# Kernel tuning notes

Measured on AMD Instinct MI355X. Metric: run time of the kernel, lower is better.

## Reference

```python
import jax, jax.numpy as jnp
import numpy as np

NUM_HEADS = 16
EMBED_DIM = 1024
HEAD_DIM = EMBED_DIM // NUM_HEADS


def setup_inputs() -> dict:
    key = jax.random.key(0)
    kq, kk, kv, kw, kb = jax.random.split(key, 5)
    B, S, D = 2, 2048, EMBED_DIM
    bound = 1.0 / np.sqrt(D)
    return {
        "query": jax.random.normal(kq, (B, S, D), dtype=jnp.float32),
        "key": jax.random.normal(kk, (B, S, D), dtype=jnp.float32),
        "value": jax.random.normal(kv, (B, S, D), dtype=jnp.float32),
        "W_out": jax.random.uniform(kw, (D, D), minval=-bound, maxval=bound, dtype=jnp.float32),
        "b_out": jax.random.uniform(kb, (D,), minval=-bound, maxval=bound, dtype=jnp.float32),
        "prelu_a": jnp.array(0.25, dtype=jnp.float32),
    }


def reference(query, key, value, W_out, b_out, prelu_a):
    B, S, D = query.shape
    # Note: the original forward never applies q/k/v linear layers, only reshape.
    q = query.reshape(B, S, NUM_HEADS, HEAD_DIM)  # b s h d
    k = key.reshape(B, S, NUM_HEADS, HEAD_DIM)
    v = value.reshape(B, S, NUM_HEADS, HEAD_DIM)
    scale = 1.0 / np.sqrt(HEAD_DIM).astype(np.float32)
    scores = jnp.einsum("bqhd,bkhd->bhqk", q, k) * scale  # [B,H,S,S]
    attn = jax.nn.softmax(scores, axis=-1)
    out = jnp.einsum("bhqk,bkhd->bqhd", attn, v).reshape(B, S, D)
    out = out @ W_out.T + b_out  # torch Linear: x @ W.T + b
    # dropout is identity in eval mode; PReLU with single scalar param
    out = jnp.where(out >= 0, out, prelu_a * out)
    return out
```

## Files before the change

kernel.cpp:

```cpp
#include <hip/hip_runtime.h>
#include <hip/hip_bf16.h>

typedef __attribute__((ext_vector_type(8))) short bf16x8;
typedef __attribute__((ext_vector_type(4))) float f32x4;

#define S_LEN 2048
#define EMB   1024
#define NH    16
#define HD    64

__device__ inline int swz(int row, int chunk) {
  return row * 64 + ((chunk ^ (row & 7)) << 3);
}

__device__ inline int swz128(int row, int chunk) {
  return row * 128 + ((chunk ^ (row & 15)) << 3);
}

__device__ inline int kperm(int s) {
  return (s & 0x23) | ((s & 0x04) << 2) | ((s & 0x18) >> 1);
}

__device__ inline uint4 cvt8(const float* __restrict__ src, float scale) {
  float4 f0 = ((const float4*)src)[0];
  float4 f1 = ((const float4*)src)[1];
  __hip_bfloat16 t[8];
  t[0] = __float2bfloat16(f0.x * scale);
  t[1] = __float2bfloat16(f0.y * scale);
  t[2] = __float2bfloat16(f0.z * scale);
  t[3] = __float2bfloat16(f0.w * scale);
  t[4] = __float2bfloat16(f1.x * scale);
  t[5] = __float2bfloat16(f1.y * scale);
  t[6] = __float2bfloat16(f1.z * scale);
  t[7] = __float2bfloat16(f1.w * scale);
  return *(uint4*)t;
}

__device__ inline uint4 cvt8r(float4 f0, float4 f1) {
  __hip_bfloat16 t[8];
  t[0] = __float2bfloat16(f0.x);
  t[1] = __float2bfloat16(f0.y);
  t[2] = __float2bfloat16(f0.z);
  t[3] = __float2bfloat16(f0.w);
  t[4] = __float2bfloat16(f1.x);
  t[5] = __float2bfloat16(f1.y);
  t[6] = __float2bfloat16(f1.z);
  t[7] = __float2bfloat16(f1.w);
  return *(uint4*)t;
}

__device__ inline void ld8f(const float* __restrict__ p, float4& a, float4& b) {
  a = ((const float4*)p)[0];
  b = ((const float4*)p)[1];
}

__global__ __launch_bounds__(256)
void prep(const float* __restrict__ K, const float* __restrict__ V,
          __hip_bfloat16* __restrict__ Kb, __hip_bfloat16* __restrict__ Vt) {
  __shared__ float vt[64 * 65];
  const int tid = threadIdx.x;
  const int st = blockIdx.x, h = blockIdx.y, b = blockIdx.z;
  const size_t srcbase = ((size_t)(b * S_LEN + st * 64)) * EMB + h * HD;
  const size_t kvb = ((size_t)(b * NH + h) * S_LEN + st * 64) * HD;
  const size_t vtb = ((size_t)(b * NH + h) * HD) * S_LEN + st * 64;

  for (int c = tid; c < 512; c += 256) {
    const int r = c >> 3, c8 = (c & 7) * 8;
    *(uint4*)(Kb + kvb + r * HD + c8) = cvt8(K + srcbase + (size_t)r * EMB + c8, 1.0f);
    const float* vsrc = V + srcbase + (size_t)r * EMB + c8;
    float4 a = ((const float4*)vsrc)[0];
    float4 d4 = ((const float4*)vsrc)[1];
    float tv[8] = {a.x, a.y, a.z, a.w, d4.x, d4.y, d4.z, d4.w};
    #pragma unroll
    for (int j = 0; j < 8; ++j) vt[r * 65 + c8 + j] = tv[j];
  }
  __syncthreads();
  for (int c = tid; c < 512; c += 256) {
    const int d = c >> 3, s8 = (c & 7) * 8;
    __hip_bfloat16 t[8];
    #pragma unroll
    for (int j = 0; j < 8; ++j)
      t[j] = __float2bfloat16(vt[(s8 + j) * 65 + d]);
    *(uint4*)(Vt + vtb + (size_t)d * S_LEN + s8) = *(uint4*)t;
  }
}

__global__ __launch_bounds__(512, 4)
void attn_fwd(const float* __restrict__ Q,
              const __hip_bfloat16* __restrict__ Kb,
              const __hip_bfloat16* __restrict__ Vt,
              __hip_bfloat16* __restrict__ O)
{
  __shared__ __align__(16) __hip_bfloat16 qs[128 * 64];
  __shared__ __align__(16) __hip_bfloat16 ks[2][128 * 64];
  __shared__ __align__(16) __hip_bfloat16 vs[2][64 * 128];

  const int qt   = blockIdx.x;
  const int h    = blockIdx.y;
  const int b    = blockIdx.z;
  const int tid  = threadIdx.x;
  const int wave = tid >> 6;
  const int lane = tid & 63;
  const int ln   = lane & 15;
  const int qd   = lane >> 4;

  const size_t baseQ = ((size_t)(b * S_LEN + qt * 128)) * EMB + h * HD;
  const size_t kvb   = ((size_t)(b * NH + h) * S_LEN) * HD;
  const size_t vtb   = ((size_t)(b * NH + h) * HD) * S_LEN;

  const int r0 = tid >> 3, cc = tid & 7;
  const int kpos0 = swz(kperm(r0), cc);
  const int kpos1 = kpos0 + 64 * 64;
  const int vr0 = tid >> 4, vch = tid & 15;
  const int vpos0 = swz128(vr0, vch);
  const int vpos1 = vpos0 + 32 * 128;

  uint4 kreg0 = *(const uint4*)(Kb + kvb + (size_t)(r0)       * HD + cc * 8);
  uint4 kreg1 = *(const uint4*)(Kb + kvb + (size_t)(64 + r0)  * HD + cc * 8);
  uint4 vreg0 = *(const uint4*)(Vt + vtb + (size_t)vr0        * S_LEN + vch * 8);
  uint4 vreg1 = *(const uint4*)(Vt + vtb + (size_t)(vr0 + 32) * S_LEN + vch * 8);

  const float qscale = 0.125f * 1.44269504088896f;
  #pragma unroll
  for (int i = 0; i < 2; ++i) {
    const int c = tid + 512 * i, row = c >> 3, ch = c & 7;
    *(uint4*)&qs[swz(row, ch)] = cvt8(Q + baseQ + (size_t)row * EMB + ch * 8, qscale);
  }
  *(uint4*)&ks[0][kpos0] = kreg0;
  *(uint4*)&ks[0][kpos1] = kreg1;
  *(uint4*)&vs[0][vpos0] = vreg0;
  *(uint4*)&vs[0][vpos1] = vreg1;
  kreg0 = *(const uint4*)(Kb + kvb + (size_t)(128 + r0)      * HD + cc * 8);
  kreg1 = *(const uint4*)(Kb + kvb + (size_t)(192 + r0)      * HD + cc * 8);
  vreg0 = *(const uint4*)(Vt + vtb + (size_t)vr0        * S_LEN + 128 + vch * 8);
  vreg1 = *(const uint4*)(Vt + vtb + (size_t)(vr0 + 32) * S_LEN + 128 + vch * 8);
  __syncthreads();

  bf16x8 aq[2];
  #pragma unroll
  for (int kh = 0; kh < 2; ++kh)
    aq[kh] = *(const bf16x8*)&qs[swz(wave * 16 + ln, kh * 4 + qd)];

  bf16x8 ones;
  #pragma unroll
  for (int j = 0; j < 8; ++j) ones[j] = (short)0x3F80;

  f32x4 oacc[4] = {};
  f32x4 lacc = {};
  bf16x8 apD[2] = {};
  bf16x8 bvD[8] = {};

  for (int kt = 0; kt < S_LEN / 128; ++kt) {
    const int cur = kt & 1;
    if (kt + 1 < S_LEN / 128) {
      *(uint4*)&ks[1 - cur][kpos0] = kreg0;
      *(uint4*)&ks[1 - cur][kpos1] = kreg1;
      *(uint4*)&vs[1 - cur][vpos0] = vreg0;
      *(uint4*)&vs[1 - cur][vpos1] = vreg1;
      if (kt + 2 < S_LEN / 128) {
        const int kb2 = (kt + 2) * 128;
        kreg0 = *(const uint4*)(Kb + kvb + (size_t)(kb2 + r0)       * HD + cc * 8);
        kreg1 = *(const uint4*)(Kb + kvb + (size_t)(kb2 + 64 + r0)  * HD + cc * 8);
        vreg0 = *(const uint4*)(Vt + vtb + (size_t)vr0        * S_LEN + kb2 + vch * 8);
        vreg1 = *(const uint4*)(Vt + vtb + (size_t)(vr0 + 32) * S_LEN + kb2 + vch * 8);
      }
    }

    f32x4 sfA[4];
    __builtin_amdgcn_s_setprio(1);
    #pragma unroll
    for (int k16 = 0; k16 < 4; ++k16) {
      const int krow = k16 * 16 + ln;
      bf16x8 ak0 = *(const bf16x8*)&ks[cur][swz(krow, qd)];
      bf16x8 ak1 = *(const bf16x8*)&ks[cur][swz(krow, 4 + qd)];
      f32x4 acc = {};
      acc = __builtin_amdgcn_mfma_f32_16x16x32_bf16(ak0, aq[0], acc, 0, 0, 0);
      sfA[k16] = __builtin_amdgcn_mfma_f32_16x16x32_bf16(ak1, aq[1], acc, 0, 0, 0);
    }
    __builtin_amdgcn_s_setprio(0);

    bf16x8 apA[2];
    #pragma unroll
    for (int t2 = 0; t2 < 2; ++t2)
      #pragma unroll
      for (int j = 0; j < 8; ++j) {
        const float p = __builtin_amdgcn_exp2f(sfA[t2 * 2 + (j >> 2)][j & 3]);
        __hip_bfloat16 hb = __float2bfloat16(p);
        apA[t2][j] = *(short*)&hb;
      }

    f32x4 sfB[4];
    __builtin_amdgcn_s_setprio(1);
    #pragma unroll
    for (int t = 0; t < 2; ++t) {
      lacc = __builtin_amdgcn_mfma_f32_16x16x32_bf16(apD[t], ones, lacc, 0, 0, 0);
      #pragma unroll
      for (int dn = 0; dn < 4; ++dn)
        oacc[dn] = __builtin_amdgcn_mfma_f32_16x16x32_bf16(apD[t], bvD[t * 4 + dn], oacc[dn], 0, 0, 0);
    }
    #pragma unroll
    for (int k16 = 0; k16 < 4; ++k16) {
      const int krow = (4 + k16) * 16 + ln;
      bf16x8 ak0 = *(const bf16x8*)&ks[cur][swz(krow, qd)];
      bf16x8 ak1 = *(const bf16x8*)&ks[cur][swz(krow, 4 + qd)];
      f32x4 acc = {};
      acc = __builtin_amdgcn_mfma_f32_16x16x32_bf16(ak0, aq[0], acc, 0, 0, 0);
      sfB[k16] = __builtin_amdgcn_mfma_f32_16x16x32_bf16(ak1, aq[1], acc, 0, 0, 0);
    }
    __builtin_amdgcn_s_setprio(0);

    bf16x8 apB[2];
    #pragma unroll
    for (int t2 = 0; t2 < 2; ++t2)
      #pragma unroll
      for (int j = 0; j < 8; ++j) {
        const float p = __builtin_amdgcn_exp2f(sfB[t2 * 2 + (j >> 2)][j & 3]);
        __hip_bfloat16 hb = __float2bfloat16(p);
        apB[t2][j] = *(short*)&hb;
      }

    __builtin_amdgcn_s_setprio(1);
    #pragma unroll
    for (int t = 0; t < 2; ++t) {
      lacc = __builtin_amdgcn_mfma_f32_16x16x32_bf16(apA[t], ones, lacc, 0, 0, 0);
      #pragma unroll
      for (int dn = 0; dn < 4; ++dn) {
        bf16x8 bv = *(const bf16x8*)&vs[cur][swz128(dn * 16 + ln, t * 4 + qd)];
        oacc[dn] = __builtin_amdgcn_mfma_f32_16x16x32_bf16(apA[t], bv, oacc[dn], 0, 0, 0);
      }
    }
    __builtin_amdgcn_s_setprio(0);

    #pragma unroll
    for (int t = 0; t < 2; ++t)
      #pragma unroll
      for (int dn = 0; dn < 4; ++dn)
        bvD[t * 4 + dn] = *(const bf16x8*)&vs[cur][swz128(dn * 16 + ln, (2 + t) * 4 + qd)];
    apD[0] = apB[0];
    apD[1] = apB[1];

    __syncthreads();
  }

  #pragma unroll
  for (int t = 0; t < 2; ++t) {
    lacc = __builtin_amdgcn_mfma_f32_16x16x32_bf16(apD[t], ones, lacc, 0, 0, 0);
    #pragma unroll
    for (int dn = 0; dn < 4; ++dn)
      oacc[dn] = __builtin_amdgcn_mfma_f32_16x16x32_bf16(apD[t], bvD[t * 4 + dn], oacc[dn], 0, 0, 0);
  }
  #pragma unroll
  for (int r = 0; r < 4; ++r) {
    const float inv = 1.f / lacc[r];
    const int row = wave * 16 + qd * 4 + r;
    #pragma unroll
    for (int dn = 0; dn < 4; ++dn)
      O[baseQ + (size_t)row * EMB + dn * 16 + ln] =
          __float2bfloat16(oacc[dn][r] * inv);
  }
}

__global__ __launch_bounds__(256, 2)
void proj_prelu(const __hip_bfloat16* __restrict__ X,
                const float* __restrict__ W,
                const float* __restrict__ Bv,
                const float* __restrict__ Pa,
                float* __restrict__ Out)
{
  __shared__ __align__(16) __hip_bfloat16 xs[2][128 * 64];
  __shared__ __align__(16) __hip_bfloat16 wsm[2][64 * 64];

  const int m0   = blockIdx.x * 128;
  const int n0   = blockIdx.y * 64;
  const int tid  = threadIdx.x;
  const int wave = tid >> 6;
  const int wm   = wave >> 1;
  const int wn   = wave & 1;
  const int lane = tid & 63;
  const int ln   = lane & 15;
  const int qd   = lane >> 4;

  const int r0 = tid >> 3, cc = tid & 7;

  f32x4 acc[8] = {};

  uint4 xg0, xg1, xg2, xg3;
  float4 wa0, wb0, wa1, wb1;
  #define LOADK(ko)                                                           \
    xg0 = *(const uint4*)(X  + (size_t)(m0 + r0     ) * EMB + (ko) + cc * 8); \
    xg1 = *(const uint4*)(X  + (size_t)(m0 + r0 + 32) * EMB + (ko) + cc * 8); \
    xg2 = *(const uint4*)(X  + (size_t)(m0 + r0 + 64) * EMB + (ko) + cc * 8); \
    xg3 = *(const uint4*)(X  + (size_t)(m0 + r0 + 96) * EMB + (ko) + cc * 8); \
    ld8f(W + (size_t)(n0 + r0     ) * EMB + (ko) + cc * 8, wa0, wb0);         \
    ld8f(W + (size_t)(n0 + r0 + 32) * EMB + (ko) + cc * 8, wa1, wb1)
  #define STORELDS(buf)                                                       \
    *(uint4*)&xs [buf][swz(r0,      cc)] = xg0;                               \
    *(uint4*)&xs [buf][swz(r0 + 32, cc)] = xg1;                               \
    *(uint4*)&xs [buf][swz(r0 + 64, cc)] = xg2;                               \
    *(uint4*)&xs [buf][swz(r0 + 96, cc)] = xg3;                               \
    *(uint4*)&wsm[buf][swz(r0,      cc)] = cvt8r(wa0, wb0);                   \
    *(uint4*)&wsm[buf][swz(r0 + 32, cc)] = cvt8r(wa1, wb1)

  LOADK(0);
  STORELDS(0);
  LOADK(64);
  __syncthreads();

  for (int kt = 0; kt < EMB / 64; ++kt) {
    const int cur = kt & 1;
    if (kt + 1 < EMB / 64) {
      STORELDS(1 - cur);
      if (kt + 2 < EMB / 64) {
        LOADK((kt + 2) * 64);
      }
    }

    #pragma unroll
    for (int ks2 = 0; ks2 < 2; ++ks2) {
      bf16x8 ax0 = *(const bf16x8*)&xs[cur][swz(wm * 64 +  0 + ln, ks2 * 4 + qd)];
      bf16x8 ax1 = *(const bf16x8*)&xs[cur][swz(wm * 64 + 16 + ln, ks2 * 4 + qd)];
      bf16x8 ax2 = *(const bf16x8*)&xs[cur][swz(wm * 64 + 32 + ln, ks2 * 4 + qd)];
      bf16x8 ax3 = *(const bf16x8*)&xs[cur][swz(wm * 64 + 48 + ln, ks2 * 4 + qd)];
      bf16x8 bw0 = *(const bf16x8*)&wsm[cur][swz(wn * 32 +  0 + ln, ks2 * 4 + qd)];
      bf16x8 bw1 = *(const bf16x8*)&wsm[cur][swz(wn * 32 + 16 + ln, ks2 * 4 + qd)];
      acc[0] = __builtin_amdgcn_mfma_f32_16x16x32_bf16(ax0, bw0, acc[0], 0, 0, 0);
      acc[1] = __builtin_amdgcn_mfma_f32_16x16x32_bf16(ax0, bw1, acc[1], 0, 0, 0);
      acc[2] = __builtin_amdgcn_mfma_f32_16x16x32_bf16(ax1, bw0, acc[2], 0, 0, 0);
      acc[3] = __builtin_amdgcn_mfma_f32_16x16x32_bf16(ax1, bw1, acc[3], 0, 0, 0);
      acc[4] = __builtin_amdgcn_mfma_f32_16x16x32_bf16(ax2, bw0, acc[4], 0, 0, 0);
      acc[5] = __builtin_amdgcn_mfma_f32_16x16x32_bf16(ax2, bw1, acc[5], 0, 0, 0);
      acc[6] = __builtin_amdgcn_mfma_f32_16x16x32_bf16(ax3, bw0, acc[6], 0, 0, 0);
      acc[7] = __builtin_amdgcn_mfma_f32_16x16x32_bf16(ax3, bw1, acc[7], 0, 0, 0);
    }
    __syncthreads();
  }

  const float a = Pa[0];
  #pragma unroll
  for (int mf = 0; mf < 4; ++mf) {
    #pragma unroll
    for (int nf = 0; nf < 2; ++nf) {
      const float bn = Bv[n0 + wn * 32 + nf * 16 + ln];
      #pragma unroll
      for (int r = 0; r < 4; ++r) {
        float y = acc[mf * 2 + nf][r] + bn;
        y = (y >= 0.f) ? y : a * y;
        Out[(size_t)(m0 + wm * 64 + mf * 16 + qd * 4 + r) * EMB +
            n0 + wn * 32 + nf * 16 + ln] = y;
      }
    }
  }
  #undef LOADK
  #undef STORELDS
}

extern "C" void kernel_launch(void* const* d_in, const int* in_sizes, int n_in,
                              void* d_out, int out_size, void* d_ws, size_t ws_size,
                              hipStream_t stream) {
  const float* Q  = (const float*)d_in[0];
  const float* K  = (const float*)d_in[1];
  const float* V  = (const float*)d_in[2];
  const float* W  = (const float*)d_in[3];
  const float* Bb = (const float*)d_in[4];
  const float* Pa = (const float*)d_in[5];
  float* Out = (float*)d_out;

  char* ws = (char*)d_ws;
  __hip_bfloat16* Xws = (__hip_bfloat16*)(ws);
  __hip_bfloat16* Kb  = (__hip_bfloat16*)(ws + (8u  << 20));
  __hip_bfloat16* Vt  = (__hip_bfloat16*)(ws + (16u << 20));

  prep      <<<dim3(S_LEN / 64, NH, 2), 256, 0, stream>>>(K, V, Kb, Vt);
  attn_fwd  <<<dim3(S_LEN / 128, NH, 2), 512, 0, stream>>>(Q, Kb, Vt, Xws);
  proj_prelu<<<dim3(2 * S_LEN / 128, EMB / 64), 256, 0, stream>>>(Xws, W, Bb, Pa, Out);
}
```

Baseline: 155.9 us.

## Fuse prep, attention and projection into one cooperative persistent kernel

Replaces the three launches with a single cooperative kernel of 512 blocks. It runs K/V conversion, then flash attention, then the output projection with PReLU, separated by grid-wide syncs, and keeps the old three-kernel path as a fallback if the cooperative launch fails. The attention loop drops the software-pipelined deferred PV stage in favour of a plain in-order schedule, and the projection retiles to 8 waves over a 128x64 tile. This aims to remove launch gaps and tail effects, but adds grid sync costs and a 512-thread projection phase with less work per wave.

```diff
diff --git a/kernel.cpp b/kernel.cpp
--- a/kernel.cpp
+++ b/kernel.cpp
@@ -1,5 +1,8 @@
 #include <hip/hip_runtime.h>
 #include <hip/hip_bf16.h>
+#include <hip/hip_cooperative_groups.h>
+
+namespace cg = cooperative_groups;
 
 typedef __attribute__((ext_vector_type(8))) short bf16x8;
 typedef __attribute__((ext_vector_type(4))) float f32x4;
@@ -54,6 +57,286 @@
   b = ((const float4*)p)[1];
 }
 
+__global__ __launch_bounds__(512, 4)
+void fused_mha(const float* __restrict__ Q, const float* __restrict__ K,
+               const float* __restrict__ V, const float* __restrict__ W,
+               const float* __restrict__ Bv, const float* __restrict__ Pa,
+               __hip_bfloat16* __restrict__ Kb, __hip_bfloat16* __restrict__ Vt,
+               __hip_bfloat16* __restrict__ X, float* __restrict__ Out)
+{
+  __shared__ __align__(16) char smem[81920];
+  cg::grid_group grid = cg::this_grid();
+
+  const int bid = blockIdx.x;
+  const int tid = threadIdx.x;
+
+  {
+    float* vt = (float*)smem;
+    #pragma unroll
+    for (int ui = 0; ui < 2; ++ui) {
+      const int u = bid + ui * 512;
+      const int st = u & 31, h = (u >> 5) & 15, b = u >> 9;
+      const size_t srcbase = ((size_t)(b * S_LEN + st * 64)) * EMB + h * HD;
+      const size_t kvbp = ((size_t)(b * NH + h) * S_LEN + st * 64) * HD;
+      const size_t vtbp = ((size_t)(b * NH + h) * HD) * S_LEN + st * 64;
+
+      const int r = tid >> 3, c8 = (tid & 7) * 8;
+      *(uint4*)(Kb + kvbp + r * HD + c8) =
+          cvt8(K + srcbase + (size_t)r * EMB + c8, 1.0f);
+      const float* vsrc = V + srcbase + (size_t)r * EMB + c8;
+      float4 a = ((const float4*)vsrc)[0];
+      float4 d4 = ((const float4*)vsrc)[1];
+      float tv[8] = {a.x, a.y, a.z, a.w, d4.x, d4.y, d4.z, d4.w};
+      #pragma unroll
+      for (int j = 0; j < 8; ++j) vt[r * 65 + c8 + j] = tv[j];
+      __syncthreads();
+      const int d = tid >> 3, s8 = (tid & 7) * 8;
+      __hip_bfloat16 t[8];
+      #pragma unroll
+      for (int j = 0; j < 8; ++j)
+        t[j] = __float2bfloat16(vt[(s8 + j) * 65 + d]);
+      *(uint4*)(Vt + vtbp + (size_t)d * S_LEN + s8) = *(uint4*)t;
+      __syncthreads();
+    }
+  }
+
+  __threadfence();
+  grid.sync();
+
+  {
+    __hip_bfloat16* qs  = (__hip_bfloat16*)smem;
+    __hip_bfloat16* ksb = (__hip_bfloat16*)(smem + 16384);
+    __hip_bfloat16* vsb = (__hip_bfloat16*)(smem + 49152);
+
+    const int qt = bid & 15;
+    const int h  = (bid >> 4) & 15;
+    const int b  = bid >> 8;
+    const int wave = tid >> 6;
+    const int lane = tid & 63;
+    const int ln   = lane & 15;
+    const int qd   = lane >> 4;
+
+    const size_t baseQ = ((size_t)(b * S_LEN + qt * 128)) * EMB + h * HD;
+    const size_t kvb   = ((size_t)(b * NH + h) * S_LEN) * HD;
+    const size_t vtb   = ((size_t)(b * NH + h) * HD) * S_LEN;
+
+    const int r0 = tid >> 3, cc = tid & 7;
+    const int kpos0 = swz(kperm(r0), cc);
+    const int kpos1 = kpos0 + 64 * 64;
+    const int vr0 = tid >> 4, vch = tid & 15;
+    const int vpos0 = swz128(vr0, vch);
+    const int vpos1 = vpos0 + 32 * 128;
+
+    uint4 kreg0 = *(const uint4*)(Kb + kvb + (size_t)(r0)       * HD + cc * 8);
+    uint4 kreg1 = *(const uint4*)(Kb + kvb + (size_t)(64 + r0)  * HD + cc * 8);
+    uint4 vreg0 = *(const uint4*)(Vt + vtb + (size_t)vr0        * S_LEN + vch * 8);
+    uint4 vreg1 = *(const uint4*)(Vt + vtb + (size_t)(vr0 + 32) * S_LEN + vch * 8);
+
+    const float qscale = 0.125f * 1.44269504088896f;
+    #pragma unroll
+    for (int i = 0; i < 2; ++i) {
+      const int c = tid + 512 * i, row = c >> 3, ch = c & 7;
+      *(uint4*)&qs[swz(row, ch)] = cvt8(Q + baseQ + (size_t)row * EMB + ch * 8, qscale);
+    }
+    *(uint4*)&ksb[kpos0] = kreg0;
+    *(uint4*)&ksb[kpos1] = kreg1;
+    *(uint4*)&vsb[vpos0] = vreg0;
+    *(uint4*)&vsb[vpos1] = vreg1;
+    kreg0 = *(const uint4*)(Kb + kvb + (size_t)(128 + r0)      * HD + cc * 8);
+    kreg1 = *(const uint4*)(Kb + kvb + (size_t)(192 + r0)      * HD + cc * 8);
+    vreg0 = *(const uint4*)(Vt + vtb + (size_t)vr0        * S_LEN + 128 + vch * 8);
+    vreg1 = *(const uint4*)(Vt + vtb + (size_t)(vr0 + 32) * S_LEN + 128 + vch * 8);
+    __syncthreads();
+
+    bf16x8 aq[2];
+    #pragma unroll
+    for (int kh = 0; kh < 2; ++kh)
+      aq[kh] = *(const bf16x8*)&qs[swz(wave * 16 + ln, kh * 4 + qd)];
+
+    bf16x8 ones;
+    #pragma unroll
+    for (int j = 0; j < 8; ++j) ones[j] = (short)0x3F80;
+
+    f32x4 oacc[4] = {};
+    f32x4 lacc = {};
+
+    for (int kt = 0; kt < S_LEN / 128; ++kt) {
+      const int cur = kt & 1;
+      __hip_bfloat16* ksc = ksb + cur * (128 * 64);
+      __hip_bfloat16* vsc = vsb + cur * (64 * 128);
+      __hip_bfloat16* ksn = ksb + (1 - cur) * (128 * 64);
+      __hip_bfloat16* vsn = vsb + (1 - cur) * (64 * 128);
+      if (kt + 1 < S_LEN / 128) {
+        *(uint4*)&ksn[kpos0] = kreg0;
+        *(uint4*)&ksn[kpos1] = kreg1;
+        *(uint4*)&vsn[vpos0] = vreg0;
+        *(uint4*)&vsn[vpos1] = vreg1;
+        if (kt + 2 < S_LEN / 128) {
+          const int kb2 = (kt + 2) * 128;
+          kreg0 = *(const uint4*)(Kb + kvb + (size_t)(kb2 + r0)       * HD + cc * 8);
+          kreg1 = *(const uint4*)(Kb + kvb + (size_t)(kb2 + 64 + r0)  * HD + cc * 8);
+          vreg0 = *(const uint4*)(Vt + vtb + (size_t)vr0        * S_LEN + kb2 + vch * 8);
+          vreg1 = *(const uint4*)(Vt + vtb + (size_t)(vr0 + 32) * S_LEN + kb2 + vch * 8);
+        }
+      }
+
+      f32x4 sfA[4], sfB[4];
+      __builtin_amdgcn_s_setprio(1);
+      #pragma unroll
+      for (int k16 = 0; k16 < 4; ++k16) {
+        const int krow = k16 * 16 + ln;
+        bf16x8 ak0 = *(const bf16x8*)&ksc[swz(krow, qd)];
+        bf16x8 ak1 = *(const bf16x8*)&ksc[swz(krow, 4 + qd)];
+        f32x4 acc = {};
+        acc = __builtin_amdgcn_mfma_f32_16x16x32_bf16(ak0, aq[0], acc, 0, 0, 0);
+        sfA[k16] = __builtin_amdgcn_mfma_f32_16x16x32_bf16(ak1, aq[1], acc, 0, 0, 0);
+      }
+      #pragma unroll
+      for (int k16 = 0; k16 < 4; ++k16) {
+        const int krow = (4 + k16) * 16 + ln;
+        bf16x8 ak0 = *(const bf16x8*)&ksc[swz(krow, qd)];
+        bf16x8 ak1 = *(const bf16x8*)&ksc[swz(krow, 4 + qd)];
+        f32x4 acc = {};
+        acc = __builtin_amdgcn_mfma_f32_16x16x32_bf16(ak0, aq[0], acc, 0, 0, 0);
+        sfB[k16] = __builtin_amdgcn_mfma_f32_16x16x32_bf16(ak1, aq[1], acc, 0, 0, 0);
+      }
+      __builtin_amdgcn_s_setprio(0);
+
+      bf16x8 apA[2];
+      #pragma unroll
+      for (int t2 = 0; t2 < 2; ++t2)
+        #pragma unroll
+        for (int j = 0; j < 8; ++j) {
+          const float p = __builtin_amdgcn_exp2f(sfA[t2 * 2 + (j >> 2)][j & 3]);
+          __hip_bfloat16 hb = __float2bfloat16(p);
+          apA[t2][j] = *(short*)&hb;
+        }
+
+      __builtin_amdgcn_s_setprio(1);
+      #pragma unroll
+      for (int t = 0; t < 2; ++t) {
+        lacc = __builtin_amdgcn_mfma_f32_16x16x32_bf16(apA[t], ones, lacc, 0, 0, 0);
+        #pragma unroll
+        for (int dn = 0; dn < 4; ++dn) {
+          bf16x8 bv = *(const bf16x8*)&vsc[swz128(dn * 16 + ln, t * 4 + qd)];
+          oacc[dn] = __builtin_amdgcn_mfma_f32_16x16x32_bf16(apA[t], bv, oacc[dn], 0, 0, 0);
+        }
+      }
+      __builtin_amdgcn_s_setprio(0);
+
+      bf16x8 apB[2];
+      #pragma unroll
+      for (int t2 = 0; t2 < 2; ++t2)
+        #pragma unroll
+        for (int j = 0; j < 8; ++j) {
+          const float p = __builtin_amdgcn_exp2f(sfB[t2 * 2 + (j >> 2)][j & 3]);
+          __hip_bfloat16 hb = __float2bfloat16(p);
+          apB[t2][j] = *(short*)&hb;
+        }
+
+      __builtin_amdgcn_s_setprio(1);
+      #pragma unroll
+      for (int t = 0; t < 2; ++t) {
+        lacc = __builtin_amdgcn_mfma_f32_16x16x32_bf16(apB[t], ones, lacc, 0, 0, 0);
+        #pragma unroll
+        for (int dn = 0; dn < 4; ++dn) {
+          bf16x8 bv = *(const bf16x8*)&vsc[swz128(dn * 16 + ln, (2 + t) * 4 + qd)];
+          oacc[dn] = __builtin_amdgcn_mfma_f32_16x16x32_bf16(apB[t], bv, oacc[dn], 0, 0, 0);
+        }
+      }
+      __builtin_amdgcn_s_setprio(0);
+
+      __syncthreads();
+    }
+
+    #pragma unroll
+    for (int r = 0; r < 4; ++r) {
+      const float inv = 1.f / lacc[r];
+      const int row = wave * 16 + qd * 4 + r;
+      #pragma unroll
+      for (int dn = 0; dn < 4; ++dn)
+        X[baseQ + (size_t)row * EMB + dn * 16 + ln] =
+            __float2bfloat16(oacc[dn][r] * inv);
+    }
+  }
+
+  __threadfence();
+  grid.sync();
+
+  {
+    __hip_bfloat16* xs  = (__hip_bfloat16*)smem;
+    __hip_bfloat16* wsm = (__hip_bfloat16*)(smem + 32768);
+
+    const int m0 = (bid & 31) * 128;
+    const int n0 = (bid >> 5) * 64;
+    const int wave = tid >> 6;
+    const int wm = wave >> 2;
+    const int wq = wave & 3;
+    const int lane = tid & 63;
+    const int ln   = lane & 15;
+    const int qd   = lane >> 4;
+    const int r0 = tid >> 3, cc = tid & 7;
+
+    f32x4 acc[4] = {};
+
+    uint4 xg0, xg1;
+    float4 wa0, wb0;
+    #define LOADK(ko)                                                            \
+      xg0 = *(const uint4*)(X + (size_t)(m0 + r0     ) * EMB + (ko) + cc * 8);   \
+      xg1 = *(const uint4*)(X + (size_t)(m0 + r0 + 64) * EMB + (ko) + cc * 8);   \
+      ld8f(W + (size_t)(n0 + r0) * EMB + (ko) + cc * 8, wa0, wb0)
+    #define STORELDS(buf)                                                        \
+      *(uint4*)&xs [(buf) * 8192 + swz(r0,      cc)] = xg0;                      \
+      *(uint4*)&xs [(buf) * 8192 + swz(r0 + 64, cc)] = xg1;                      \
+      *(uint4*)&wsm[(buf) * 4096 + swz(r0,      cc)] = cvt8r(wa0, wb0)
+
+    LOADK(0);
+    STORELDS(0);
+    LOADK(64);
+    __syncthreads();
+
+    for (int kt = 0; kt < EMB / 64; ++kt) {
+      const int cur = kt & 1;
+      if (kt + 1 < EMB / 64) {
+        STORELDS(1 - cur);
+        if (kt + 2 < EMB / 64) {
+          LOADK((kt + 2) * 64);
+        }
+      }
+      const __hip_bfloat16* xc = xs + cur * 8192;
+      const __hip_bfloat16* wc = wsm + cur * 4096;
+      #pragma unroll
+      for (int ks2 = 0; ks2 < 2; ++ks2) {
+        bf16x8 ax0 = *(const bf16x8*)&xc[swz(wm * 64 +  0 + ln, ks2 * 4 + qd)];
+        bf16x8 ax1 = *(const bf16x8*)&xc[swz(wm * 64 + 16 + ln, ks2 * 4 + qd)];
+        bf16x8 ax2 = *(const bf16x8*)&xc[swz(wm * 64 + 32 + ln, ks2 * 4 + qd)];
+        bf16x8 ax3 = *(const bf16x8*)&xc[swz(wm * 64 + 48 + ln, ks2 * 4 + qd)];
+        bf16x8 bw  = *(const bf16x8*)&wc[swz(wq * 16 + ln, ks2 * 4 + qd)];
+        acc[0] = __builtin_amdgcn_mfma_f32_16x16x32_bf16(ax0, bw, acc[0], 0, 0, 0);
+        acc[1] = __builtin_amdgcn_mfma_f32_16x16x32_bf16(ax1, bw, acc[1], 0, 0, 0);
+        acc[2] = __builtin_amdgcn_mfma_f32_16x16x32_bf16(ax2, bw, acc[2], 0, 0, 0);
+        acc[3] = __builtin_amdgcn_mfma_f32_16x16x32_bf16(ax3, bw, acc[3], 0, 0, 0);
+      }
+      __syncthreads();
+    }
+
+    const float a = Pa[0];
+    const float bn = Bv[n0 + wq * 16 + ln];
+    #pragma unroll
+    for (int mf = 0; mf < 4; ++mf) {
+      #pragma unroll
+      for (int r = 0; r < 4; ++r) {
+        float y = acc[mf][r] + bn;
+        y = (y >= 0.f) ? y : a * y;
+        Out[(size_t)(m0 + wm * 64 + mf * 16 + qd * 4 + r) * EMB +
+            n0 + wq * 16 + ln] = y;
+      }
+    }
+    #undef LOADK
+    #undef STORELDS
+  }
+}
+
 __global__ __launch_bounds__(256)
 void prep(const float* __restrict__ K, const float* __restrict__ V,
           __hip_bfloat16* __restrict__ Kb, __hip_bfloat16* __restrict__ Vt) {
@@ -95,14 +378,9 @@
   __shared__ __align__(16) __hip_bfloat16 ks[2][128 * 64];
   __shared__ __align__(16) __hip_bfloat16 vs[2][64 * 128];
 
-  const int qt   = blockIdx.x;
-  const int h    = blockIdx.y;
-  const int b    = blockIdx.z;
-  const int tid  = threadIdx.x;
-  const int wave = tid >> 6;
-  const int lane = tid & 63;
-  const int ln   = lane & 15;
-  const int qd   = lane >> 4;
+  const int qt = blockIdx.x, h = blockIdx.y, b = blockIdx.z;
+  const int tid = threadIdx.x;
+  const int wave = tid >> 6, lane = tid & 63, ln = lane & 15, qd = lane >> 4;
 
   const size_t baseQ = ((size_t)(b * S_LEN + qt * 128)) * EMB + h * HD;
   const size_t kvb   = ((size_t)(b * NH + h) * S_LEN) * HD;
@@ -147,8 +425,6 @@
 
   f32x4 oacc[4] = {};
   f32x4 lacc = {};
-  bf16x8 apD[2] = {};
-  bf16x8 bvD[8] = {};
 
   for (int kt = 0; kt < S_LEN / 128; ++kt) {
     const int cur = kt & 1;
@@ -166,7 +442,7 @@
       }
     }
 
-    f32x4 sfA[4];
+    f32x4 sfA[4], sfB[4];
     __builtin_amdgcn_s_setprio(1);
     #pragma unroll
     for (int k16 = 0; k16 < 4; ++k16) {
@@ -177,27 +453,6 @@
       acc = __builtin_amdgcn_mfma_f32_16x16x32_bf16(ak0, aq[0], acc, 0, 0, 0);
       sfA[k16] = __builtin_amdgcn_mfma_f32_16x16x32_bf16(ak1, aq[1], acc, 0, 0, 0);
     }
-    __builtin_amdgcn_s_setprio(0);
-
-    bf16x8 apA[2];
-    #pragma unroll
-    for (int t2 = 0; t2 < 2; ++t2)
-      #pragma unroll
-      for (int j = 0; j < 8; ++j) {
-        const float p = __builtin_amdgcn_exp2f(sfA[t2 * 2 + (j >> 2)][j & 3]);
-        __hip_bfloat16 hb = __float2bfloat16(p);
-        apA[t2][j] = *(short*)&hb;
-      }
-
-    f32x4 sfB[4];
-    __builtin_amdgcn_s_setprio(1);
-    #pragma unroll
-    for (int t = 0; t < 2; ++t) {
-      lacc = __builtin_amdgcn_mfma_f32_16x16x32_bf16(apD[t], ones, lacc, 0, 0, 0);
-      #pragma unroll
-      for (int dn = 0; dn < 4; ++dn)
-        oacc[dn] = __builtin_amdgcn_mfma_f32_16x16x32_bf16(apD[t], bvD[t * 4 + dn], oacc[dn], 0, 0, 0);
-    }
     #pragma unroll
     for (int k16 = 0; k16 < 4; ++k16) {
       const int krow = (4 + k16) * 16 + ln;
@@ -209,6 +464,28 @@
     }
     __builtin_amdgcn_s_setprio(0);
 
+    bf16x8 apA[2];
+    #pragma unroll
+    for (int t2 = 0; t2 < 2; ++t2)
+      #pragma unroll
+      for (int j = 0; j < 8; ++j) {
+        const float p = __builtin_amdgcn_exp2f(sfA[t2 * 2 + (j >> 2)][j & 3]);
+        __hip_bfloat16 hb = __float2bfloat16(p);
+        apA[t2][j] = *(short*)&hb;
+      }
+
+    __builtin_amdgcn_s_setprio(1);
+    #pragma unroll
+    for (int t = 0; t < 2; ++t) {
+      lacc = __builtin_amdgcn_mfma_f32_16x16x32_bf16(apA[t], ones, lacc, 0, 0, 0);
+      #pragma unroll
+      for (int dn = 0; dn < 4; ++dn) {
+        bf16x8 bv = *(const bf16x8*)&vs[cur][swz128(dn * 16 + ln, t * 4 + qd)];
+        oacc[dn] = __builtin_amdgcn_mfma_f32_16x16x32_bf16(apA[t], bv, oacc[dn], 0, 0, 0);
+      }
+    }
+    __builtin_amdgcn_s_setprio(0);
+
     bf16x8 apB[2];
     #pragma unroll
     for (int t2 = 0; t2 < 2; ++t2)
@@ -222,33 +499,18 @@
     __builtin_amdgcn_s_setprio(1);
     #pragma unroll
     for (int t = 0; t < 2; ++t) {
-      lacc = __builtin_amdgcn_mfma_f32_16x16x32_bf16(apA[t], ones, lacc, 0, 0, 0);
+      lacc = __builtin_amdgcn_mfma_f32_16x16x32_bf16(apB[t], ones, lacc, 0, 0, 0);
       #pragma unroll
       for (int dn = 0; dn < 4; ++dn) {
-        bf16x8 bv = *(const bf16x8*)&vs[cur][swz128(dn * 16 + ln, t * 4 + qd)];
-        oacc[dn] = __builtin_amdgcn_mfma_f32_16x16x32_bf16(apA[t], bv, oacc[dn], 0, 0, 0);
+        bf16x8 bv = *(const bf16x8*)&vs[cur][swz128(dn * 16 + ln, (2 + t) * 4 + qd)];
+        oacc[dn] = __builtin_amdgcn_mfma_f32_16x16x32_bf16(apB[t], bv, oacc[dn], 0, 0, 0);
       }
     }
     __builtin_amdgcn_s_setprio(0);
 
-    #pragma unroll
-    for (int t = 0; t < 2; ++t)
-      #pragma unroll
-      for (int dn = 0; dn < 4; ++dn)
-        bvD[t * 4 + dn] = *(const bf16x8*)&vs[cur][swz128(dn * 16 + ln, (2 + t) * 4 + qd)];
-    apD[0] = apB[0];
-    apD[1] = apB[1];
-
     __syncthreads();
   }
 
-  #pragma unroll
-  for (int t = 0; t < 2; ++t) {
-    lacc = __builtin_amdgcn_mfma_f32_16x16x32_bf16(apD[t], ones, lacc, 0, 0, 0);
-    #pragma unroll
-    for (int dn = 0; dn < 4; ++dn)
-      oacc[dn] = __builtin_amdgcn_mfma_f32_16x16x32_bf16(apD[t], bvD[t * 4 + dn], oacc[dn], 0, 0, 0);
-  }
   #pragma unroll
   for (int r = 0; r < 4; ++r) {
     const float inv = 1.f / lacc[r];
@@ -270,16 +532,12 @@
   __shared__ __align__(16) __hip_bfloat16 xs[2][128 * 64];
   __shared__ __align__(16) __hip_bfloat16 wsm[2][64 * 64];
 
-  const int m0   = blockIdx.x * 128;
-  const int n0   = blockIdx.y * 64;
-  const int tid  = threadIdx.x;
+  const int m0 = blockIdx.x * 128;
+  const int n0 = blockIdx.y * 64;
+  const int tid = threadIdx.x;
   const int wave = tid >> 6;
-  const int wm   = wave >> 1;
-  const int wn   = wave & 1;
-  const int lane = tid & 63;
-  const int ln   = lane & 15;
-  const int qd   = lane >> 4;
-
+  const int wm = wave >> 1, wn = wave & 1;
+  const int lane = tid & 63, ln = lane & 15, qd = lane >> 4;
   const int r0 = tid >> 3, cc = tid & 7;
 
   f32x4 acc[8] = {};
@@ -314,7 +572,6 @@
         LOADK((kt + 2) * 64);
       }
     }
-
     #pragma unroll
     for (int ks2 = 0; ks2 < 2; ++ks2) {
       bf16x8 ax0 = *(const bf16x8*)&xs[cur][swz(wm * 64 +  0 + ln, ks2 * 4 + qd)];
@@ -370,7 +627,15 @@
   __hip_bfloat16* Kb  = (__hip_bfloat16*)(ws + (8u  << 20));
   __hip_bfloat16* Vt  = (__hip_bfloat16*)(ws + (16u << 20));
 
-  prep      <<<dim3(S_LEN / 64, NH, 2), 256, 0, stream>>>(K, V, Kb, Vt);
-  attn_fwd  <<<dim3(S_LEN / 128, NH, 2), 512, 0, stream>>>(Q, Kb, Vt, Xws);
-  proj_prelu<<<dim3(2 * S_LEN / 128, EMB / 64), 256, 0, stream>>>(Xws, W, Bb, Pa, Out);
-}
+  void* kargs[] = {(void*)&Q, (void*)&K, (void*)&V, (void*)&W, (void*)&Bb,
+                   (void*)&Pa, (void*)&Kb, (void*)&Vt, (void*)&Xws, (void*)&Out};
+  hipError_t err = hipLaunchCooperativeKernel(
+      reinterpret_cast<const void*>(&fused_mha),
+      dim3(512), dim3(512), kargs, 0, stream);
+
+  if (err != hipSuccess) {
+    prep      <<<dim3(S_LEN / 64, NH, 2), 256, 0, stream>>>(K, V, Kb, Vt);
+    attn_fwd  <<<dim3(S_LEN / 128, NH, 2), 512, 0, stream>>>(Q, Kb, Vt, Xws);
+    proj_prelu<<<dim3(2 * S_LEN / 128, EMB / 64), 256, 0, stream>>>(Xws, W, Bb, Pa, Out);
+  }
+}
```

Result: slower. 488.7 us (+213.5%).
